# Kernel tuning notes

Measured on AMD Instinct MI355X. Metric: run time of the kernel, lower is better.

Reference implementation:

```python
import jax, jax.numpy as jnp
import numpy as np

T = 2_000_000  # timesteps


def setup_inputs() -> dict:
    key = jax.random.key(0)
    u = jax.random.normal(key, (T, 2), dtype=jnp.float32) * 10.0  # external forces per step
    x0 = jnp.zeros((4,), dtype=jnp.float32)  # [z1, v1, z2, v2]
    c = jnp.array([10.0, 10.0, 10.0], dtype=jnp.float32)   # trainable damping c1,c2,c3
    m = jnp.array([20.0, 10.0], dtype=jnp.float32)          # masses m1,m2 (frozen)
    k = jnp.array([2.0e3, 1.0e3, 5.0e3], dtype=jnp.float32) # stiffness k1,k2,k3 (frozen)
    dt = jnp.float32(0.002)
    return {"u": u, "x0": x0, "c": c, "m": m, "k": k, "dt": dt}


def reference(u, x0, c, m, k, dt):
    c1, c2, c3 = c[0], c[1], c[2]
    m1, m2 = m[0], m[1]
    k1, k2, k3 = k[0], k[1], k[2]

    def deriv(x, ut):
        # x = [z1, v1, z2, v2]; returns dx/dt = [v1, a1, v2, a2]
        z1, v1, z2, v2 = x[0], x[1], x[2], x[3]
        a1 = (ut[0] - (c1 + c2) * v1 + c2 * v2 - (k1 + k2) * z1 + k2 * z2) / m1
        a2 = (ut[1] - (c3 + c2) * v2 + c2 * v1 - (k3 + k2) * z2 + k2 * z1) / m2
        return jnp.stack([v1, a1, v2, a2])

    half = dt * 0.5

    def step(x, ut):
        s1 = deriv(x, ut)
        s2 = deriv(x + half * s1, ut)
        s3 = deriv(x + half * s2, ut)
        s4 = deriv(x + dt * s3, ut)
        xn = x + (dt / 6.0) * (s1 + 2.0 * s2 + 2.0 * s3 + s4)
        y = jnp.stack([xn[0], xn[2]])  # positions z1, z2 (matches cell output)
        return xn, y

    _, ys = jax.lax.scan(step, x0, u)
    return ys  # [T, 2]
```

## Files before the change

### kernel.cpp

```cpp
#include <hip/hip_runtime.h>

#define BLK 256
#define LS  16
#define SPB (BLK*LS)
#define STR (LS+1)

#define WS_AGG 0
#define WS_S1  2048

#define STEP4(Mx,Nx, s0,s1,s2,s3, ux,uy, n0,n1,n2,n3)                                              \
  n0 = fmaf(Mx[0],s0,  fmaf(Mx[1],s1,  fmaf(Mx[2],s2,  fmaf(Mx[3],s3,  fmaf(Nx[0],ux, Nx[1]*uy))))); \
  n1 = fmaf(Mx[4],s0,  fmaf(Mx[5],s1,  fmaf(Mx[6],s2,  fmaf(Mx[7],s3,  fmaf(Nx[2],ux, Nx[3]*uy))))); \
  n2 = fmaf(Mx[8],s0,  fmaf(Mx[9],s1,  fmaf(Mx[10],s2, fmaf(Mx[11],s3, fmaf(Nx[4],ux, Nx[5]*uy))))); \
  n3 = fmaf(Mx[12],s0, fmaf(Mx[13],s1, fmaf(Mx[14],s2, fmaf(Mx[15],s3, fmaf(Nx[6],ux, Nx[7]*uy)))));

__device__ __forceinline__ float4 aff_apply(const float* Mx, float4 l, float4 c) {
  float4 r;
  r.x = fmaf(Mx[0],l.x,  fmaf(Mx[1],l.y,  fmaf(Mx[2],l.z,  fmaf(Mx[3],l.w,  c.x))));
  r.y = fmaf(Mx[4],l.x,  fmaf(Mx[5],l.y,  fmaf(Mx[6],l.z,  fmaf(Mx[7],l.w,  c.y))));
  r.z = fmaf(Mx[8],l.x,  fmaf(Mx[9],l.y,  fmaf(Mx[10],l.z, fmaf(Mx[11],l.w, c.z))));
  r.w = fmaf(Mx[12],l.x, fmaf(Mx[13],l.y, fmaf(Mx[14],l.z, fmaf(Mx[15],l.w, c.w))));
  return r;
}

__device__ __forceinline__ float4 matvec(const float* Mx, float4 v) {
  return aff_apply(Mx, v, make_float4(0.f, 0.f, 0.f, 0.f));
}

__device__ __forceinline__ double mm_el(double x, double y, int i, int j) {
  double s = 0.0;
  #pragma unroll
  for (int l = 0; l < 4; ++l)
    s = fma(__shfl(x, 4*i + l, 64), __shfl(y, 4*l + j, 64), s);
  return s;
}

__device__ __forceinline__ void wave_setup(const float* __restrict__ cin,
                                           const float* __restrict__ min_,
                                           const float* __restrict__ kin,
                                           const float* __restrict__ dtin,
                                           float* Ms, float* Ns, float* SKs, float* GKs,
                                           int lane, bool wantGK) {
  double c1 = cin[0], c2 = cin[1], c3 = cin[2];
  double m1 = min_[0], m2 = min_[1];
  double k1 = kin[0], k2 = kin[1], k3 = kin[2];
  double h  = dtin[0];
  const int i = (lane >> 2) & 3, j = lane & 3;

  double a;
  if (i == 0)      a = (j == 1) ? 1.0 : 0.0;
  else if (i == 2) a = (j == 3) ? 1.0 : 0.0;
  else if (i == 1) a = (j==0) ? -(k1+k2)/m1 : (j==1) ? -(c1+c2)/m1
                     : (j==2) ?  k2/m1      :  c2/m1;
  else             a = (j==0) ?  k2/m2      : (j==1) ?  c2/m2
                     : (j==2) ? -(k3+k2)/m2 : -(c3+c2)/m2;

  const double id = (i == j) ? 1.0 : 0.0;
  double q  = id + (h/4.0)*a;
  double t  = mm_el(a, q,  i, j);
  double r  = id + (h/3.0)*t;
  t         = mm_el(a, r,  i, j);
  double s_ = id + (h/2.0)*t;
  t         = mm_el(a, s_, i, j);
  double m  = id + h*t;
  if (lane < 16) Ms[lane] = (float)m;

  {
    int e = lane & 7, ii = e >> 1, jp = e & 1, col = jp ? 3 : 1;
    double sv = __shfl(s_, 4*ii + col, 64);
    double nv = h * sv / (jp ? m2 : m1);
    if (lane < 8) Ns[lane] = (float)nv;
  }

  double p = m;
  #pragma unroll
  for (int rr = 0; rr < 4; ++rr) p = mm_el(p, p, i, j);
  if (lane < 16) SKs[lane] = (float)p;
  #pragma unroll
  for (int k = 1; k < 8; ++k) {
    p = mm_el(p, p, i, j);
    if (lane < 16) SKs[16*k + lane] = (float)p;
  }
  if (wantGK) {
    p = mm_el(p, p, i, j);
    if (lane < 16) GKs[lane] = (float)p;
    #pragma unroll
    for (int k = 1; k < 9; ++k) {
      p = mm_el(p, p, i, j);
      if (lane < 16) GKs[16*k + lane] = (float)p;
    }
  }
}

__launch_bounds__(BLK)
__global__ void k_pass1(const float4* __restrict__ u4,
                        const float* __restrict__ cc, const float* __restrict__ mmp,
                        const float* __restrict__ kp, const float* __restrict__ dtp,
                        float4* __restrict__ s1out, float4* __restrict__ agg, int T2) {
  __shared__ float  uxp[BLK*STR];
  __shared__ float  uyp[BLK*STR];
  __shared__ float4 S1[BLK];
  __shared__ float  Ms[16], Ns[8], SKs[8*16];
  const int tid   = threadIdx.x;
  const int bid   = blockIdx.x;
  const int base2 = bid * SPB;

  if (tid < 64) wave_setup(cc, mmp, kp, dtp, Ms, Ns, SKs, nullptr, tid, false);

  #pragma unroll
  for (int kk = 0; kk < SPB/2/BLK; ++kk) {
    int idx4 = tid + kk*BLK;
    int s0 = 2*idx4;
    float4 v = make_float4(0.f, 0.f, 0.f, 0.f);
    if (base2 + s0 < T2) v = u4[(base2 >> 1) + idx4];
    int t0 = s0 >> 4, j0 = s0 & 15;
    int t1 = (s0+1) >> 4, j1 = (s0+1) & 15;
    uxp[t0*STR + j0] = v.x;  uyp[t0*STR + j0] = v.y;
    uxp[t1*STR + j1] = v.z;  uyp[t1*STR + j1] = v.w;
  }
  __syncthreads();

  float Mm[16], Nn[8];
  #pragma unroll
  for (int i = 0; i < 16; ++i) Mm[i] = Ms[i];
  #pragma unroll
  for (int i = 0; i < 8;  ++i) Nn[i] = Ns[i];

  float b0 = 0.f, b1 = 0.f, b2 = 0.f, b3 = 0.f;
  #pragma unroll
  for (int j = 0; j < LS; ++j) {
    float ux = uxp[tid*STR + j], uy = uyp[tid*STR + j];
    float n0, n1, n2, n3;
    STEP4(Mm, Nn, b0, b1, b2, b3, ux, uy, n0, n1, n2, n3);
    b0 = n0; b1 = n1; b2 = n2; b3 = n3;
  }
  S1[tid] = make_float4(b0, b1, b2, b3);
  __syncthreads();

  #pragma unroll
  for (int k = 0; k < 8; ++k) {
    int off = 1 << k;
    float4 l, c;
    bool act = (tid >= off);
    if (act) { l = S1[tid - off]; c = S1[tid]; }
    __syncthreads();
    if (act) S1[tid] = aff_apply(&SKs[16*k], l, c);
    __syncthreads();
  }

  s1out[bid * BLK + tid] = S1[tid];
  if (tid == BLK-1) agg[bid] = S1[BLK-1];
}

__launch_bounds__(BLK)
__global__ void k_pass3(const float4* __restrict__ u4,
                        const float* __restrict__ cc, const float* __restrict__ mmp,
                        const float* __restrict__ kp, const float* __restrict__ dtp,
                        const float4* __restrict__ s1buf, const float4* __restrict__ agg,
                        const float* __restrict__ x0in, float4* __restrict__ out4,
                        int T2, int nblk) {
  __shared__ float  uxp[BLK*STR];
  __shared__ float  uyp[BLK*STR];
  __shared__ float4 MA[512];
  __shared__ float4 MB[512];
  __shared__ float  Ms[16], Ns[8], SKs[8*16], GKs[9*16];
  const int tid   = threadIdx.x;
  const int bid   = blockIdx.x;
  const int base2 = bid * SPB;

  if (tid < 64) wave_setup(cc, mmp, kp, dtp, Ms, Ns, SKs, GKs, tid, true);

  #pragma unroll
  for (int kk = 0; kk < SPB/2/BLK; ++kk) {
    int idx4 = tid + kk*BLK;
    int s0 = 2*idx4;
    float4 v = make_float4(0.f, 0.f, 0.f, 0.f);
    if (base2 + s0 < T2) v = u4[(base2 >> 1) + idx4];
    int t0 = s0 >> 4, j0 = s0 & 15;
    int t1 = (s0+1) >> 4, j1 = (s0+1) & 15;
    uxp[t0*STR + j0] = v.x;  uyp[t0*STR + j0] = v.y;
    uxp[t1*STR + j1] = v.z;  uyp[t1*STR + j1] = v.w;
  }

  const int n = nblk + 1;
  #pragma unroll
  for (int j = 0; j < 2; ++j) {
    int i = tid + BLK*j;
    if (i < n) MA[i] = (i == 0) ? make_float4(x0in[0], x0in[1], x0in[2], x0in[3])
                                : agg[i-1];
  }
  __syncthreads();

  float Mm[16], Nn[8];
  #pragma unroll
  for (int i = 0; i < 16; ++i) Mm[i] = Ms[i];
  #pragma unroll
  for (int i = 0; i < 8;  ++i) Nn[i] = Ns[i];

  float4* Aa = MA; float4* Bb = MB;
  for (int k = 0; k < 9; ++k) {
    int off = 1 << k;
    if (off >= n) break;
    #pragma unroll
    for (int j = 0; j < 2; ++j) {
      int i = tid + BLK*j;
      if (i < n) {
        float4 v = Aa[i];
        if (i >= off) v = aff_apply(&GKs[16*k], Aa[i-off], v);
        Bb[i] = v;
      }
    }
    __syncthreads();
    float4* t = Aa; Aa = Bb; Bb = t;
  }

  float4 Xbs = Aa[bid];

  float4 v = Xbs;
  #pragma unroll
  for (int k = 0; k < 8; ++k)
    if (tid & (1 << k)) v = matvec(&SKs[16*k], v);
  float4 p = (tid > 0) ? s1buf[bid*BLK + tid - 1] : make_float4(0.f, 0.f, 0.f, 0.f);
  float x0 = v.x + p.x, x1 = v.y + p.y, x2 = v.z + p.z, x3 = v.w + p.w;

  #pragma unroll
  for (int j = 0; j < LS; ++j) {
    float ux = uxp[tid*STR + j], uy = uyp[tid*STR + j];
    float n0, n1, n2, n3;
    STEP4(Mm, Nn, x0, x1, x2, x3, ux, uy, n0, n1, n2, n3);
    x0 = n0; x1 = n1; x2 = n2; x3 = n3;
    uxp[tid*STR + j] = x0;
    uyp[tid*STR + j] = x2;
  }
  __syncthreads();

  #pragma unroll
  for (int kk = 0; kk < SPB/2/BLK; ++kk) {
    int idx4 = tid + kk*BLK;
    int s0 = 2*idx4;
    if (base2 + s0 < T2) {
      int t0 = s0 >> 4, j0 = s0 & 15;
      int t1 = (s0+1) >> 4, j1 = (s0+1) & 15;
      out4[(base2 >> 1) + idx4] = make_float4(uxp[t0*STR + j0], uyp[t0*STR + j0],
                                              uxp[t1*STR + j1], uyp[t1*STR + j1]);
    }
  }
}

extern "C" void kernel_launch(void* const* d_in, const int* in_sizes, int n_in,
                              void* d_out, int out_size, void* d_ws, size_t ws_size,
                              hipStream_t stream) {
  const float* u   = (const float*)d_in[0];
  const float* x0  = (const float*)d_in[1];
  const float* cc  = (const float*)d_in[2];
  const float* mm  = (const float*)d_in[3];
  const float* kk  = (const float*)d_in[4];
  const float* dt  = (const float*)d_in[5];

  const int T2   = in_sizes[0] / 2;
  const int nblk = (T2 + SPB - 1) / SPB;

  float*  ws  = (float*)d_ws;
  float4* agg = (float4*)(ws + WS_AGG);
  float4* s1b = (float4*)(ws + WS_S1);

  k_pass1<<<nblk, BLK, 0, stream>>>((const float4*)u, cc, mm, kk, dt, s1b, agg, T2);
  k_pass3<<<nblk, BLK, 0, stream>>>((const float4*)u, cc, mm, kk, dt, s1b, agg, x0,
                                    (float4*)d_out, T2, nblk);
}
```

Measured before the change: 95.32 us.

## Replace shared-memory block scan with wave shuffle scan and recompute partials in pass3

```diff
diff --git a/kernel.cpp b/kernel.cpp
--- a/kernel.cpp
+++ b/kernel.cpp
@@ -5,8 +5,12 @@
 #define SPB (BLK*LS)
 #define STR (LS+1)
 
-#define WS_AGG 0
-#define WS_S1  2048
+#define WC_M   0
+#define WC_N   16
+#define WC_SK  24
+#define WC_GK  152
+#define WC_TOT 296
+#define WS_AGG 320
 
 #define STEP4(Mx,Nx, s0,s1,s2,s3, ux,uy, n0,n1,n2,n3)                                              \
   n0 = fmaf(Mx[0],s0,  fmaf(Mx[1],s1,  fmaf(Mx[2],s2,  fmaf(Mx[3],s3,  fmaf(Nx[0],ux, Nx[1]*uy))))); \
@@ -27,6 +31,11 @@
   return aff_apply(Mx, v, make_float4(0.f, 0.f, 0.f, 0.f));
 }
 
+__device__ __forceinline__ float4 shfl_up4(float4 v, int d) {
+  return make_float4(__shfl_up(v.x, d, 64), __shfl_up(v.y, d, 64),
+                     __shfl_up(v.z, d, 64), __shfl_up(v.w, d, 64));
+}
+
 __device__ __forceinline__ double mm_el(double x, double y, int i, int j) {
   double s = 0.0;
   #pragma unroll
@@ -39,8 +48,7 @@
                                            const float* __restrict__ min_,
                                            const float* __restrict__ kin,
                                            const float* __restrict__ dtin,
-                                           float* Ms, float* Ns, float* SKs, float* GKs,
-                                           int lane, bool wantGK) {
+                                           float* C, int lane, bool wantGK) {
   double c1 = cin[0], c2 = cin[1], c3 = cin[2];
   double m1 = min_[0], m2 = min_[1];
   double k1 = kin[0], k2 = kin[1], k3 = kin[2];
@@ -63,49 +71,71 @@
   double s_ = id + (h/2.0)*t;
   t         = mm_el(a, s_, i, j);
   double m  = id + h*t;
-  if (lane < 16) Ms[lane] = (float)m;
+  if (lane < 16) C[WC_M + lane] = (float)m;
 
   {
     int e = lane & 7, ii = e >> 1, jp = e & 1, col = jp ? 3 : 1;
     double sv = __shfl(s_, 4*ii + col, 64);
     double nv = h * sv / (jp ? m2 : m1);
-    if (lane < 8) Ns[lane] = (float)nv;
+    if (lane < 8) C[WC_N + lane] = (float)nv;
   }
 
   double p = m;
   #pragma unroll
   for (int rr = 0; rr < 4; ++rr) p = mm_el(p, p, i, j);
-  if (lane < 16) SKs[lane] = (float)p;
+  if (lane < 16) C[WC_SK + lane] = (float)p;
   #pragma unroll
   for (int k = 1; k < 8; ++k) {
     p = mm_el(p, p, i, j);
-    if (lane < 16) SKs[16*k + lane] = (float)p;
+    if (lane < 16) C[WC_SK + 16*k + lane] = (float)p;
   }
   if (wantGK) {
     p = mm_el(p, p, i, j);
-    if (lane < 16) GKs[lane] = (float)p;
+    if (lane < 16) C[WC_GK + lane] = (float)p;
     #pragma unroll
     for (int k = 1; k < 9; ++k) {
       p = mm_el(p, p, i, j);
-      if (lane < 16) GKs[16*k + lane] = (float)p;
+      if (lane < 16) C[WC_GK + 16*k + lane] = (float)p;
     }
   }
+}
+
+__device__ __forceinline__ float4 wave_scan(const float* SK, float4 b, int lane) {
+  float4 cur = b;
+  #pragma unroll
+  for (int k = 0; k < 6; ++k) {
+    int off = 1 << k;
+    float4 l  = shfl_up4(cur, off);
+    float4 nv = aff_apply(&SK[16*k], l, cur);
+    if (lane >= off) cur = nv;
+  }
+  return cur;
+}
+
+__device__ __forceinline__ float4 cross_wave_excl(const float* SK, const float4* Wagg, int w) {
+  float4 E = make_float4(0.f, 0.f, 0.f, 0.f);
+  if (w > 0) {
+    E = Wagg[0];
+    for (int q = 1; q < w; ++q) E = aff_apply(&SK[16*6], E, Wagg[q]);
+  }
+  return E;
 }
 
 __launch_bounds__(BLK)
 __global__ void k_pass1(const float4* __restrict__ u4,
                         const float* __restrict__ cc, const float* __restrict__ mmp,
                         const float* __restrict__ kp, const float* __restrict__ dtp,
-                        float4* __restrict__ s1out, float4* __restrict__ agg, int T2) {
+                        float* __restrict__ wsc, float4* __restrict__ agg, int T2) {
   __shared__ float  uxp[BLK*STR];
   __shared__ float  uyp[BLK*STR];
-  __shared__ float4 S1[BLK];
-  __shared__ float  Ms[16], Ns[8], SKs[8*16];
+  __shared__ float  C[WC_TOT];
+  __shared__ float4 Wagg[4];
   const int tid   = threadIdx.x;
   const int bid   = blockIdx.x;
+  const int lane  = tid & 63, w = tid >> 6;
   const int base2 = bid * SPB;
 
-  if (tid < 64) wave_setup(cc, mmp, kp, dtp, Ms, Ns, SKs, nullptr, tid, false);
+  if (tid < 64) wave_setup(cc, mmp, kp, dtp, C, tid, bid == 0);
 
   #pragma unroll
   for (int kk = 0; kk < SPB/2/BLK; ++kk) {
@@ -120,11 +150,15 @@
   }
   __syncthreads();
 
+  if (bid == 0)
+    for (int i = tid; i < WC_TOT; i += BLK) wsc[i] = C[i];
+
   float Mm[16], Nn[8];
   #pragma unroll
-  for (int i = 0; i < 16; ++i) Mm[i] = Ms[i];
-  #pragma unroll
-  for (int i = 0; i < 8;  ++i) Nn[i] = Ns[i];
+  for (int i = 0; i < 16; ++i) Mm[i] = C[WC_M+i];
+  #pragma unroll
+  for (int i = 0; i < 8;  ++i) Nn[i] = C[WC_N+i];
+  const float* SK = &C[WC_SK];
 
   float b0 = 0.f, b1 = 0.f, b2 = 0.f, b3 = 0.f;
   #pragma unroll
@@ -134,41 +168,36 @@
     STEP4(Mm, Nn, b0, b1, b2, b3, ux, uy, n0, n1, n2, n3);
     b0 = n0; b1 = n1; b2 = n2; b3 = n3;
   }
-  S1[tid] = make_float4(b0, b1, b2, b3);
+
+  float4 incl = wave_scan(SK, make_float4(b0, b1, b2, b3), lane);
+  if (lane == 63) Wagg[w] = incl;
   __syncthreads();
 
-  #pragma unroll
-  for (int k = 0; k < 8; ++k) {
-    int off = 1 << k;
-    float4 l, c;
-    bool act = (tid >= off);
-    if (act) { l = S1[tid - off]; c = S1[tid]; }
-    __syncthreads();
-    if (act) S1[tid] = aff_apply(&SKs[16*k], l, c);
-    __syncthreads();
-  }
-
-  s1out[bid * BLK + tid] = S1[tid];
-  if (tid == BLK-1) agg[bid] = S1[BLK-1];
+  if (tid == BLK-1) {
+    float4 E = cross_wave_excl(SK, Wagg, 3);
+    float4 t_ = matvec(&SK[16*6], E);
+    agg[bid] = make_float4(incl.x + t_.x, incl.y + t_.y, incl.z + t_.z, incl.w + t_.w);
+  }
 }
 
 __launch_bounds__(BLK)
 __global__ void k_pass3(const float4* __restrict__ u4,
-                        const float* __restrict__ cc, const float* __restrict__ mmp,
-                        const float* __restrict__ kp, const float* __restrict__ dtp,
-                        const float4* __restrict__ s1buf, const float4* __restrict__ agg,
+                        const float* __restrict__ wsc,
+                        const float4* __restrict__ agg,
                         const float* __restrict__ x0in, float4* __restrict__ out4,
                         int T2, int nblk) {
   __shared__ float  uxp[BLK*STR];
   __shared__ float  uyp[BLK*STR];
   __shared__ float4 MA[512];
   __shared__ float4 MB[512];
-  __shared__ float  Ms[16], Ns[8], SKs[8*16], GKs[9*16];
+  __shared__ float  C[WC_TOT];
+  __shared__ float4 Wagg[4];
   const int tid   = threadIdx.x;
   const int bid   = blockIdx.x;
+  const int lane  = tid & 63, w = tid >> 6;
   const int base2 = bid * SPB;
 
-  if (tid < 64) wave_setup(cc, mmp, kp, dtp, Ms, Ns, SKs, GKs, tid, true);
+  for (int i = tid; i < WC_TOT; i += BLK) C[i] = wsc[i];
 
   #pragma unroll
   for (int kk = 0; kk < SPB/2/BLK; ++kk) {
@@ -193,9 +222,22 @@
 
   float Mm[16], Nn[8];
   #pragma unroll
-  for (int i = 0; i < 16; ++i) Mm[i] = Ms[i];
-  #pragma unroll
-  for (int i = 0; i < 8;  ++i) Nn[i] = Ns[i];
+  for (int i = 0; i < 16; ++i) Mm[i] = C[WC_M+i];
+  #pragma unroll
+  for (int i = 0; i < 8;  ++i) Nn[i] = C[WC_N+i];
+  const float* SK = &C[WC_SK];
+  const float* GK = &C[WC_GK];
+
+  float b0 = 0.f, b1 = 0.f, b2 = 0.f, b3 = 0.f;
+  #pragma unroll
+  for (int j = 0; j < LS; ++j) {
+    float ux = uxp[tid*STR + j], uy = uyp[tid*STR + j];
+    float n0, n1, n2, n3;
+    STEP4(Mm, Nn, b0, b1, b2, b3, ux, uy, n0, n1, n2, n3);
+    b0 = n0; b1 = n1; b2 = n2; b3 = n3;
+  }
+  float4 incl = wave_scan(SK, make_float4(b0, b1, b2, b3), lane);
+  if (lane == 63) Wagg[w] = incl;
 
   float4* Aa = MA; float4* Bb = MB;
   for (int k = 0; k < 9; ++k) {
@@ -206,7 +248,7 @@
       int i = tid + BLK*j;
       if (i < n) {
         float4 v = Aa[i];
-        if (i >= off) v = aff_apply(&GKs[16*k], Aa[i-off], v);
+        if (i >= off) v = aff_apply(&GK[16*k], Aa[i-off], v);
         Bb[i] = v;
       }
     }
@@ -216,12 +258,19 @@
 
   float4 Xbs = Aa[bid];
 
-  float4 v = Xbs;
-  #pragma unroll
-  for (int k = 0; k < 8; ++k)
-    if (tid & (1 << k)) v = matvec(&SKs[16*k], v);
-  float4 p = (tid > 0) ? s1buf[bid*BLK + tid - 1] : make_float4(0.f, 0.f, 0.f, 0.f);
-  float x0 = v.x + p.x, x1 = v.y + p.y, x2 = v.z + p.z, x3 = v.w + p.w;
+  float4 E  = cross_wave_excl(SK, Wagg, w);
+  float4 Xw = Xbs;
+  if (w & 1) Xw = matvec(&SK[16*6], Xw);
+  if (w & 2) Xw = matvec(&SK[16*7], Xw);
+  Xw = make_float4(Xw.x + E.x, Xw.y + E.y, Xw.z + E.z, Xw.w + E.w);
+
+  float4 ex = shfl_up4(incl, 1);
+  if (lane == 0) ex = make_float4(0.f, 0.f, 0.f, 0.f);
+  float4 v = Xw;
+  #pragma unroll
+  for (int k = 0; k < 6; ++k)
+    if (lane & (1 << k)) v = matvec(&SK[16*k], v);
+  float x0 = v.x + ex.x, x1 = v.y + ex.y, x2 = v.z + ex.z, x3 = v.w + ex.w;
 
   #pragma unroll
   for (int j = 0; j < LS; ++j) {
@@ -262,9 +311,8 @@
 
   float*  ws  = (float*)d_ws;
   float4* agg = (float4*)(ws + WS_AGG);
-  float4* s1b = (float4*)(ws + WS_S1);
-
-  k_pass1<<<nblk, BLK, 0, stream>>>((const float4*)u, cc, mm, kk, dt, s1b, agg, T2);
-  k_pass3<<<nblk, BLK, 0, stream>>>((const float4*)u, cc, mm, kk, dt, s1b, agg, x0,
+
+  k_pass1<<<nblk, BLK, 0, stream>>>((const float4*)u, cc, mm, kk, dt, ws, agg, T2);
+  k_pass3<<<nblk, BLK, 0, stream>>>((const float4*)u, ws, agg, x0,
                                     (float4*)d_out, T2, nblk);
 }
```

Result: no change. 94.86 us (-0.5%).
